# Optimization experiments

Hardware: AMD Instinct MI355X
Metric: run time of the kernel (lower is better)

## Reference

```python
import jax, jax.numpy as jnp
import numpy as np

EMBED_PHI = 1024
EMBED_F = 1024
HIDDEN_F = 1024
N_HEADS = 16
B, S = 2, 2048


def setup_inputs() -> dict:
    key = jax.random.key(0)
    ks = jax.random.split(key, 9)
    sphi = 1.0 / np.sqrt(EMBED_PHI)
    sf = 1.0 / np.sqrt(EMBED_F)
    sh = 1.0 / np.sqrt(HIDDEN_F)
    return {
        "q": jax.random.normal(ks[0], (B, S, EMBED_PHI), jnp.float32),
        "k": jax.random.normal(ks[1], (B, S, EMBED_PHI), jnp.float32),
        "v": jax.random.normal(ks[2], (B, S, EMBED_F), jnp.float32),
        "Wq": jax.random.normal(ks[3], (HIDDEN_F, EMBED_PHI), jnp.float32) * sphi,
        "Wk": jax.random.normal(ks[4], (HIDDEN_F, EMBED_PHI), jnp.float32) * sphi,
        "Wv": jax.random.normal(ks[5], (HIDDEN_F, EMBED_F), jnp.float32) * sf,
        "bv": jax.random.normal(ks[6], (HIDDEN_F,), jnp.float32) * sf,
        "Wo": jax.random.normal(ks[7], (EMBED_F, HIDDEN_F), jnp.float32) * sh,
        "bo": jax.random.normal(ks[8], (EMBED_F,), jnp.float32) * sh,
    }


def reference(q, k, v, Wq, Wk, Wv, bv, Wo, bo):
    Bq, Sq, _ = q.shape
    hd = HIDDEN_F // N_HEADS
    scale = 1.0 / np.sqrt(hd)
    # projections; torch Linear: y = x @ W.T + b
    qh = (q @ Wq.T).reshape(Bq, Sq, N_HEADS, hd).transpose(0, 2, 1, 3)  # [B,H,S,d]
    kh = (k @ Wk.T).reshape(Bq, Sq, N_HEADS, hd).transpose(0, 2, 1, 3)
    vh = (v @ Wv.T + bv).reshape(Bq, Sq, N_HEADS, hd).transpose(0, 2, 1, 3)
    scores = jnp.einsum("bhsd,bhtd->bhst", qh, kh) * scale  # [B,H,S,S]
    # mask: triu(diagonal=0) masked (attend strictly to past) except [0,0] unmasked
    mask = jnp.triu(jnp.ones((Sq, Sq), dtype=bool), k=0).at[0, 0].set(False)
    scores = jnp.where(mask, -jnp.inf, scores)
    probs = jax.nn.softmax(scores, axis=-1)  # dropout is identity at eval
    out = jnp.einsum("bhst,bhtd->bhsd", probs, vh)
    out = out.transpose(0, 2, 1, 3).reshape(Bq, Sq, HIDDEN_F)
    return out @ Wo.T + bo
```

## Files before the change

### kernel.cpp

```cpp
#include <hip/hip_runtime.h>
#include <hip/hip_bf16.h>

typedef __attribute__((ext_vector_type(8))) short short8;
typedef __attribute__((ext_vector_type(4))) float f32x4;
typedef __attribute__((ext_vector_type(4))) unsigned short us4;
typedef __attribute__((ext_vector_type(2))) unsigned int u32x2;

#define NE  1024
#define SEQ 2048

__device__ __forceinline__ float bf2f(unsigned short u) {
    union { unsigned u; float f; } x; x.u = ((unsigned)u) << 16; return x.f;
}
__device__ __forceinline__ unsigned short f2bf(float f) {
    union { float f; unsigned u; } x; x.f = f;
    unsigned r = x.u + 0x7FFFu + ((x.u >> 16) & 1u);
    return (unsigned short)(r >> 16);
}
__device__ __forceinline__ unsigned short f2bf_fast(float f) {
    union { float f; unsigned u; } x; x.f = f;
    return (unsigned short)((x.u + 0x8000u) >> 16);
}

__global__ void detect_dtype(const unsigned short* __restrict__ s,
                             int* __restrict__ flag) {
    __shared__ int cnt;
    const int t = threadIdx.x;
    if (t == 0) cnt = 0;
    __syncthreads();
    unsigned short u = s[t];
    int e = (u >> 7) & 0xFF;
    int sane = (e == 0) || (e >= 100 && e <= 140);
    atomicAdd(&cnt, sane);
    __syncthreads();
    if (t == 0) flag[0] = (cnt >= 230) ? 1 : 0;
}

struct Ptrs7 { const void* s[7]; unsigned short* d[7]; };

__global__ void convert7(Ptrs7 p, const int* __restrict__ flag, int zoff) {
    const int z = blockIdx.z + zoff;
    const int n = (z < 3) ? (4 << 20) : (1 << 20);
    const bool in_f32 = (flag[0] == 0);
    unsigned short* d = p.d[z];
    const int stride = gridDim.x * blockDim.x;
    for (int i8 = blockIdx.x * blockDim.x + threadIdx.x; i8 * 8 < n; i8 += stride) {
        size_t off = (size_t)i8 * 8;
        if (in_f32) {
            const float* sp = (const float*)p.s[z] + off;
            float4 a = *(const float4*)sp, b2 = *(const float4*)(sp + 4);
            short8 sv;
            sv[0] = (short)f2bf(a.x);  sv[1] = (short)f2bf(a.y);
            sv[2] = (short)f2bf(a.z);  sv[3] = (short)f2bf(a.w);
            sv[4] = (short)f2bf(b2.x); sv[5] = (short)f2bf(b2.y);
            sv[6] = (short)f2bf(b2.z); sv[7] = (short)f2bf(b2.w);
            *(short8*)(d + off) = sv;
        } else {
            *(short8*)(d + off) = *(const short8*)((const unsigned short*)p.s[z] + off);
        }
    }
}

template<int AWS, int WWS, int OUTF, int VT>
__global__ __launch_bounds__(256, 3)
void gemm_bt(const void* A0, const void* A1, const void* A2,
             const void* W0, const void* W1, const void* W2,
             const void* b0, const void* b1, const void* b2,
             void* C0, void* C1, void* C2,
             const int* __restrict__ flag)
{
    __shared__ __align__(16) unsigned short As[128 * 32];
    __shared__ __align__(16) unsigned short Bs[128 * 32];
    const int z = blockIdx.z;
    const void* Ap = (z == 0) ? A0 : (z == 1) ? A1 : A2;
    const void* Wp = (z == 0) ? W0 : (z == 1) ? W1 : W2;
    const void* bp = (z == 0) ? b0 : (z == 1) ? b1 : b2;
    void*       Cp = (z == 0) ? C0 : (z == 1) ? C1 : C2;
    const bool in_f32 = (flag[0] == 0);
    const int t = threadIdx.x;
    const int w = t >> 6, l = t & 63, q = l >> 4, n = l & 15;
    const int m0 = blockIdx.y * 128, n0 = blockIdx.x * 128;
    const int wm = (w >> 1) * 64, wn = (w & 1) * 64;
    const int srow = t >> 2, sk = (t & 3) * 8;

    f32x4 acc[4][4] = {};

    for (int k0 = 0; k0 < NE; k0 += 32) {
        if (AWS || !in_f32) {
            #pragma unroll
            for (int hh = 0; hh < 2; hh++) {
                const unsigned short* ga = (const unsigned short*)Ap +
                    (size_t)(m0 + srow + hh * 64) * NE + k0 + sk;
                __builtin_amdgcn_global_load_lds(
                    (const __attribute__((address_space(1))) void*)ga,
                    (__attribute__((address_space(3))) void*)&As[hh * 2048 + w * 512],
                    16, 0, 0);
            }
        } else {
            #pragma unroll
            for (int hh = 0; hh < 2; hh++) {
                const float* a = (const float*)Ap +
                                 (size_t)(m0 + srow + hh * 64) * NE + k0 + sk;
                float4 x0 = *(const float4*)a, x1 = *(const float4*)(a + 4);
                short8 sv;
                sv[0] = (short)f2bf(x0.x); sv[1] = (short)f2bf(x0.y);
                sv[2] = (short)f2bf(x0.z); sv[3] = (short)f2bf(x0.w);
                sv[4] = (short)f2bf(x1.x); sv[5] = (short)f2bf(x1.y);
                sv[6] = (short)f2bf(x1.z); sv[7] = (short)f2bf(x1.w);
                *(short8*)(&As[hh * 2048 + t * 8]) = sv;
            }
        }
        if (WWS || !in_f32) {
            #pragma unroll
            for (int hh = 0; hh < 2; hh++) {
                const unsigned short* ga = (const unsigned short*)Wp +
                    (size_t)(n0 + srow + hh * 64) * NE + k0 + sk;
                __builtin_amdgcn_global_load_lds(
                    (const __attribute__((address_space(1))) void*)ga,
                    (__attribute__((address_space(3))) void*)&Bs[hh * 2048 + w * 512],
                    16, 0, 0);
            }
        } else {
            #pragma unroll
            for (int hh = 0; hh < 2; hh++) {
                const float* a = (const float*)Wp +
                                 (size_t)(n0 + srow + hh * 64) * NE + k0 + sk;
                float4 x0 = *(const float4*)a, x1 = *(const float4*)(a + 4);
                short8 sv;
                sv[0] = (short)f2bf(x0.x); sv[1] = (short)f2bf(x0.y);
                sv[2] = (short)f2bf(x0.z); sv[3] = (short)f2bf(x0.w);
                sv[4] = (short)f2bf(x1.x); sv[5] = (short)f2bf(x1.y);
                sv[6] = (short)f2bf(x1.z); sv[7] = (short)f2bf(x1.w);
                *(short8*)(&Bs[hh * 2048 + t * 8]) = sv;
            }
        }
        __syncthreads();

        short8 af[4], bfv[4];
        #pragma unroll
        for (int mt = 0; mt < 4; mt++)
            af[mt] = *(const short8*)(&As[(wm + mt * 16 + n) * 32 + q * 8]);
        #pragma unroll
        for (int nt = 0; nt < 4; nt++)
            bfv[nt] = *(const short8*)(&Bs[(wn + nt * 16 + n) * 32 + q * 8]);
        #pragma unroll
        for (int mt = 0; mt < 4; mt++)
            #pragma unroll
            for (int nt = 0; nt < 4; nt++)
                acc[mt][nt] = __builtin_amdgcn_mfma_f32_16x16x32_bf16(
                    af[mt], bfv[nt], acc[mt][nt], 0, 0, 0);
        __syncthreads();
    }

    #pragma unroll
    for (int mt = 0; mt < 4; mt++)
        #pragma unroll
        for (int nt = 0; nt < 4; nt++) {
            int row0 = m0 + wm + mt * 16 + q * 4;
            int col  = n0 + wn + nt * 16 + n;
            float bia = 0.f;
            if (bp)
                bia = in_f32 ? ((const float*)bp)[col]
                             : bf2f(((const unsigned short*)bp)[col]);
            if (VT && z == 2) {
                int bb = row0 >> 11, s0 = row0 & 2047;
                int hh2 = col >> 6, dd = col & 63;
                us4 pk4;
                #pragma unroll
                for (int r = 0; r < 4; r++)
                    pk4[r] = f2bf(acc[mt][nt][r] + bia);
                *(us4*)((unsigned short*)Cp +
                        ((size_t)((bb * 16 + hh2) * 64 + dd) << 11) + s0) = pk4;
            } else {
                #pragma unroll
                for (int r = 0; r < 4; r++) {
                    float v2 = acc[mt][nt][r] + bia;
                    size_t idx = (size_t)(row0 + r) * NE + col;
                    if (OUTF && in_f32) ((float*)Cp)[idx] = v2;
                    else                ((unsigned short*)Cp)[idx] = f2bf(v2);
                }
            }
        }
}

__global__ __launch_bounds__(512, 4)
void attn(const unsigned short* qh, const unsigned short* kh,
          const unsigned short* vt, unsigned short* ctx)
{
    __shared__ __align__(16) unsigned short Ks[2][64 * 72];
    __shared__ __align__(16) unsigned short Vt[2][64 * 72];
    __shared__ __align__(16) unsigned short Ps[8][16 * 72];
    const int t = threadIdx.x, w = t >> 6, l = t & 63;
    const int q = l >> 4, n = l & 15;
    const int half = w >> 2, sub = w & 3;
    const int h = blockIdx.y, b = blockIdx.z;
    const int pair = b ? (15 - blockIdx.x) : blockIdx.x;
    const int qbB = pair, qbA = 31 - pair;
    const int qb = half ? qbB : qbA;
    const size_t base = (size_t)b * SEQ * NE + h * 64;
    const size_t vbase = (size_t)((b * 16 + h) * 64) << 11;
    const int i0 = qb * 64 + sub * 16;

    short8 qf[2];
    qf[0] = *(const short8*)(&qh[base + (size_t)(i0 + n) * NE + q * 8]);
    qf[1] = *(const short8*)(&qh[base + (size_t)(i0 + n) * NE + 32 + q * 8]);

    f32x4 o[4] = {};
    float lsp[4] = {0.f, 0.f, 0.f, 0.f};

    const float K1 = 0.125f * 1.4426950408889634f;
    const float B2 = 24.0f * 1.4426950408889634f;

    const int kr = t >> 3, kc = (t & 7) * 8;
    const int vd = t >> 3, vj = (t & 7) * 8;

    short8 pk, pv;
    pk = *(const short8*)(&kh[base + (size_t)kr * NE + kc]);
    pv = *(const short8*)(&vt[vbase + ((size_t)vd << 11) + vj]);
    *(short8*)(&Ks[0][kr * 72 + kc]) = pk;
    *(short8*)(&Vt[0][vd * 72 + vj]) = pv;
    if (qbA >= 1) {
        pk = *(const short8*)(&kh[base + (size_t)(64 + kr) * NE + kc]);
        pv = *(const short8*)(&vt[vbase + ((size_t)vd << 11) + 64 + vj]);
    }
    __syncthreads();

    unsigned short* PsW = &Ps[w][0];
    int cur = 0;

    for (int jt = 0; jt <= qbA; jt++) {
        if (jt + 1 <= qbA) {
            *(short8*)(&Ks[cur ^ 1][kr * 72 + kc]) = pk;
            *(short8*)(&Vt[cur ^ 1][vd * 72 + vj]) = pv;
        }
        if (jt + 2 <= qbA) {
            const int jn = (jt + 2) * 64;
            pk = *(const short8*)(&kh[base + (size_t)(jn + kr) * NE + kc]);
            pv = *(const short8*)(&vt[vbase + ((size_t)vd << 11) + jn + vj]);
        }

        if (jt <= qb) {
            const unsigned short* Kc = &Ks[cur][0];
            const unsigned short* Vc = &Vt[cur][0];
            f32x4 sa[4] = {};
            __builtin_amdgcn_s_setprio(1);
            #pragma unroll
            for (int ks = 0; ks < 2; ks++)
                #pragma unroll
                for (int nt = 0; nt < 4; nt++) {
                    short8 kf = *(const short8*)(&Kc[(nt * 16 + n) * 72 + ks * 32 + q * 8]);
                    sa[nt] = __builtin_amdgcn_mfma_f32_16x16x32_bf16(kf, qf[ks], sa[nt], 0, 0, 0);
                }
            __builtin_amdgcn_s_setprio(0);

            const bool diag = (jt == qb);
            const int i = i0 + n;
            #pragma unroll
            for (int nt = 0; nt < 4; nt++) {
                float p[4];
                #pragma unroll
                for (int r = 0; r < 4; r++) {
                    float e = fmaf(sa[nt][r], K1, -B2);
                    if (diag) {
                        int j = jt * 64 + nt * 16 + q * 4 + r;
                        bool ok = (j < i) || (i == 0 && j == 0);
                        e = ok ? e : -256.0f;
                    }
                    p[r] = __builtin_amdgcn_exp2f(e);
                }
                lsp[nt] += (p[0] + p[1]) + (p[2] + p[3]);
                unsigned w0, w1;
                asm("v_cvt_pk_bf16_f32 %0, %1, %2" : "=v"(w0) : "v"(p[0]), "v"(p[1]));
                asm("v_cvt_pk_bf16_f32 %0, %1, %2" : "=v"(w1) : "v"(p[2]), "v"(p[3]));
                u32x2 wv; wv[0] = w0; wv[1] = w1;
                *(u32x2*)(&PsW[n * 72 + nt * 16 + q * 4]) = wv;
            }
            asm volatile("s_waitcnt lgkmcnt(0)" ::: "memory");

            #pragma unroll
            for (int ks = 0; ks < 2; ks++) {
                short8 pf = *(const short8*)(&PsW[n * 72 + ks * 32 + q * 8]);
                __builtin_amdgcn_s_setprio(1);
                #pragma unroll
                for (int dt = 0; dt < 4; dt++) {
                    short8 vf = *(const short8*)(&Vc[(dt * 16 + n) * 72 + ks * 32 + q * 8]);
                    o[dt] = __builtin_amdgcn_mfma_f32_16x16x32_bf16(pf, vf, o[dt], 0, 0, 0);
                }
                __builtin_amdgcn_s_setprio(0);
            }
        }
        __syncthreads();
        cur ^= 1;
    }

    float ls = (lsp[0] + lsp[1]) + (lsp[2] + lsp[3]);
    ls += __shfl_xor(ls, 16, 64);
    ls += __shfl_xor(ls, 32, 64);

    #pragma unroll
    for (int r = 0; r < 4; r++) {
        float inv = 1.0f / __shfl(ls, q * 4 + r, 64);
        #pragma unroll
        for (int dt = 0; dt < 4; dt++)
            ctx[base + (size_t)(i0 + q * 4 + r) * NE + dt * 16 + n] =
                f2bf(o[dt][r] * inv);
    }
}

extern "C" void kernel_launch(void* const* d_in, const int* in_sizes, int n_in,
                              void* d_out, int out_size, void* d_ws, size_t ws_size,
                              hipStream_t stream) {
    const void* q  = d_in[0];
    const void* k  = d_in[1];
    const void* v  = d_in[2];
    const void* Wq = d_in[3];
    const void* Wk = d_in[4];
    const void* Wv = d_in[5];
    const void* bv = d_in[6];
    const void* Wo = d_in[7];
    const void* bo = d_in[8];

    const size_t MB = 1024 * 1024;
    const size_t M4 = 4 * MB;
    unsigned short* ws = (unsigned short*)d_ws;
    unsigned short* qh  = ws;
    unsigned short* kh  = ws + 1 * M4;
    unsigned short* vt  = ws + 2 * M4;
    unsigned short* ctx = qh;

    int tier = (ws_size >= 56 * MB + 64) ? 2 : (ws_size >= 32 * MB + 64) ? 1 : 0;

    unsigned short *qc, *kc, *vc, *Wqc, *Wkc, *Wvc, *Woc;
    int* flag;
    if (tier == 2) {
        qc = ws + 3 * M4; kc = ws + 4 * M4; vc = ws + 5 * M4;
        Wqc = ws + 6 * M4;           Wkc = Wqc + 1 * MB;
        Wvc = Wqc + 2 * MB;          Woc = Wqc + 3 * MB;
        flag = (int*)((char*)d_ws + 56 * MB);
    } else if (tier == 1) {
        qc = kc = vc = nullptr;
        Wqc = ws + 3 * M4;           Wkc = Wqc + 1 * MB;
        Wvc = Wqc + 2 * MB;          Woc = Wqc + 3 * MB;
        flag = (int*)((char*)d_ws + 32 * MB);
    } else {
        qc = kc = vc = nullptr; Wqc = Wkc = Wvc = Woc = nullptr;
        flag = (int*)((char*)d_ws + 24 * MB);
    }

    detect_dtype<<<1, 256, 0, stream>>>((const unsigned short*)q, flag);

    if (tier > 0) {
        Ptrs7 p;
        p.s[0] = q;  p.s[1] = k;  p.s[2] = v;
        p.s[3] = Wq; p.s[4] = Wk; p.s[5] = Wv; p.s[6] = Wo;
        p.d[0] = qc; p.d[1] = kc; p.d[2] = vc;
        p.d[3] = Wqc; p.d[4] = Wkc; p.d[5] = Wvc; p.d[6] = Woc;
        if (tier == 2)
            convert7<<<dim3(512, 1, 7), 256, 0, stream>>>(p, flag, 0);
        else
            convert7<<<dim3(512, 1, 4), 256, 0, stream>>>(p, flag, 3);
    }

    if (tier == 2)
        gemm_bt<1, 1, 0, 1><<<dim3(8, 32, 3), 256, 0, stream>>>(
            qc, kc, vc, Wqc, Wkc, Wvc, nullptr, nullptr, bv, qh, kh, vt, flag);
    else if (tier == 1)
        gemm_bt<0, 1, 0, 1><<<dim3(8, 32, 3), 256, 0, stream>>>(
            q, k, v, Wqc, Wkc, Wvc, nullptr, nullptr, bv, qh, kh, vt, flag);
    else
        gemm_bt<0, 0, 0, 1><<<dim3(8, 32, 3), 256, 0, stream>>>(
            q, k, v, Wq, Wk, Wv, nullptr, nullptr, bv, qh, kh, vt, flag);

    attn<<<dim3(16, 16, 2), 512, 0, stream>>>(qh, kh, vt, ctx);

    if (tier > 0)
        gemm_bt<1, 1, 1, 0><<<dim3(8, 32, 1), 256, 0, stream>>>(
            ctx, ctx, ctx, Woc, Woc, Woc, bo, bo, bo, d_out, d_out, d_out, flag);
    else
        gemm_bt<1, 0, 1, 0><<<dim3(8, 32, 1), 256, 0, stream>>>(
            ctx, ctx, ctx, Wo, Wo, Wo, bo, bo, bo, d_out, d_out, d_out, flag);
}
```

Before: 228.4 us.

## Software-pipeline attention PV MFMAs and narrow output GEMM tile to 64 columns

In the attention kernel, each iteration now preloads its K fragments up front and defers the P·V MFMAs to the next iteration. The previous tile's P and V fragments are held in registers, so those MFMAs can overlap the next score computation and softmax. A flush runs at jt == qb+1 for the shorter half and after the loop for the longer half. The output projection GEMM gets a TN template parameter and launches with 64-wide N tiles, doubling the block count to fill more CUs. The cost is extra register pressure from the held fragments and less reuse of the A tile in the output GEMM.

```diff
diff --git a/kernel.cpp b/kernel.cpp
--- a/kernel.cpp
+++ b/kernel.cpp
@@ -61,7 +61,7 @@
     }
 }
 
-template<int AWS, int WWS, int OUTF, int VT>
+template<int AWS, int WWS, int OUTF, int VT, int TN = 128>
 __global__ __launch_bounds__(256, 3)
 void gemm_bt(const void* A0, const void* A1, const void* A2,
              const void* W0, const void* W1, const void* W2,
@@ -69,8 +69,9 @@
              void* C0, void* C1, void* C2,
              const int* __restrict__ flag)
 {
+    constexpr int NT = TN / 32;
     __shared__ __align__(16) unsigned short As[128 * 32];
-    __shared__ __align__(16) unsigned short Bs[128 * 32];
+    __shared__ __align__(16) unsigned short Bs[TN * 32];
     const int z = blockIdx.z;
     const void* Ap = (z == 0) ? A0 : (z == 1) ? A1 : A2;
     const void* Wp = (z == 0) ? W0 : (z == 1) ? W1 : W2;
@@ -79,11 +80,11 @@
     const bool in_f32 = (flag[0] == 0);
     const int t = threadIdx.x;
     const int w = t >> 6, l = t & 63, q = l >> 4, n = l & 15;
-    const int m0 = blockIdx.y * 128, n0 = blockIdx.x * 128;
-    const int wm = (w >> 1) * 64, wn = (w & 1) * 64;
+    const int m0 = blockIdx.y * 128, n0 = blockIdx.x * TN;
+    const int wm = (w >> 1) * 64, wn = (w & 1) * (TN / 2);
     const int srow = t >> 2, sk = (t & 3) * 8;
 
-    f32x4 acc[4][4] = {};
+    f32x4 acc[4][NT] = {};
 
     for (int k0 = 0; k0 < NE; k0 += 32) {
         if (AWS || !in_f32) {
@@ -112,7 +113,7 @@
         }
         if (WWS || !in_f32) {
             #pragma unroll
-            for (int hh = 0; hh < 2; hh++) {
+            for (int hh = 0; hh < TN / 64; hh++) {
                 const unsigned short* ga = (const unsigned short*)Wp +
                     (size_t)(n0 + srow + hh * 64) * NE + k0 + sk;
                 __builtin_amdgcn_global_load_lds(
@@ -122,7 +123,7 @@
             }
         } else {
             #pragma unroll
-            for (int hh = 0; hh < 2; hh++) {
+            for (int hh = 0; hh < TN / 64; hh++) {
                 const float* a = (const float*)Wp +
                                  (size_t)(n0 + srow + hh * 64) * NE + k0 + sk;
                 float4 x0 = *(const float4*)a, x1 = *(const float4*)(a + 4);
@@ -136,17 +137,17 @@
         }
         __syncthreads();
 
-        short8 af[4], bfv[4];
+        short8 af[4], bfv[NT];
         #pragma unroll
         for (int mt = 0; mt < 4; mt++)
             af[mt] = *(const short8*)(&As[(wm + mt * 16 + n) * 32 + q * 8]);
         #pragma unroll
-        for (int nt = 0; nt < 4; nt++)
+        for (int nt = 0; nt < NT; nt++)
             bfv[nt] = *(const short8*)(&Bs[(wn + nt * 16 + n) * 32 + q * 8]);
         #pragma unroll
         for (int mt = 0; mt < 4; mt++)
             #pragma unroll
-            for (int nt = 0; nt < 4; nt++)
+            for (int nt = 0; nt < NT; nt++)
                 acc[mt][nt] = __builtin_amdgcn_mfma_f32_16x16x32_bf16(
                     af[mt], bfv[nt], acc[mt][nt], 0, 0, 0);
         __syncthreads();
@@ -155,7 +156,7 @@
     #pragma unroll
     for (int mt = 0; mt < 4; mt++)
         #pragma unroll
-        for (int nt = 0; nt < 4; nt++) {
+        for (int nt = 0; nt < NT; nt++) {
             int row0 = m0 + wm + mt * 16 + q * 4;
             int col  = n0 + wn + nt * 16 + n;
             float bia = 0.f;
@@ -207,6 +208,8 @@
 
     f32x4 o[4] = {};
     float lsp[4] = {0.f, 0.f, 0.f, 0.f};
+    short8 pf_prev[2];
+    short8 vf_prev[8];
 
     const float K1 = 0.125f * 1.4426950408889634f;
     const float B2 = 24.0f * 1.4426950408889634f;
@@ -242,15 +245,33 @@
         if (jt <= qb) {
             const unsigned short* Kc = &Ks[cur][0];
             const unsigned short* Vc = &Vt[cur][0];
+
+            short8 kf[2][4];
+            #pragma unroll
+            for (int ks = 0; ks < 2; ks++)
+                #pragma unroll
+                for (int nt = 0; nt < 4; nt++)
+                    kf[ks][nt] = *(const short8*)(&Kc[(nt * 16 + n) * 72 + ks * 32 + q * 8]);
+
+            if (jt > 0) {
+                __builtin_amdgcn_s_setprio(1);
+                #pragma unroll
+                for (int ks = 0; ks < 2; ks++)
+                    #pragma unroll
+                    for (int dt = 0; dt < 4; dt++)
+                        o[dt] = __builtin_amdgcn_mfma_f32_16x16x32_bf16(
+                            pf_prev[ks], vf_prev[ks * 4 + dt], o[dt], 0, 0, 0);
+                __builtin_amdgcn_s_setprio(0);
+            }
+
             f32x4 sa[4] = {};
             __builtin_amdgcn_s_setprio(1);
             #pragma unroll
             for (int ks = 0; ks < 2; ks++)
                 #pragma unroll
-                for (int nt = 0; nt < 4; nt++) {
-                    short8 kf = *(const short8*)(&Kc[(nt * 16 + n) * 72 + ks * 32 + q * 8]);
-                    sa[nt] = __builtin_amdgcn_mfma_f32_16x16x32_bf16(kf, qf[ks], sa[nt], 0, 0, 0);
-                }
+                for (int nt = 0; nt < 4; nt++)
+                    sa[nt] = __builtin_amdgcn_mfma_f32_16x16x32_bf16(
+                        kf[ks][nt], qf[ks], sa[nt], 0, 0, 0);
             __builtin_amdgcn_s_setprio(0);
 
             const bool diag = (jt == qb);
@@ -278,19 +299,35 @@
             asm volatile("s_waitcnt lgkmcnt(0)" ::: "memory");
 
             #pragma unroll
-            for (int ks = 0; ks < 2; ks++) {
-                short8 pf = *(const short8*)(&PsW[n * 72 + ks * 32 + q * 8]);
-                __builtin_amdgcn_s_setprio(1);
-                #pragma unroll
-                for (int dt = 0; dt < 4; dt++) {
-                    short8 vf = *(const short8*)(&Vc[(dt * 16 + n) * 72 + ks * 32 + q * 8]);
-                    o[dt] = __builtin_amdgcn_mfma_f32_16x16x32_bf16(pf, vf, o[dt], 0, 0, 0);
-                }
-                __builtin_amdgcn_s_setprio(0);
-            }
+            for (int ks = 0; ks < 2; ks++)
+                pf_prev[ks] = *(const short8*)(&PsW[n * 72 + ks * 32 + q * 8]);
+            #pragma unroll
+            for (int ks = 0; ks < 2; ks++)
+                #pragma unroll
+                for (int dt = 0; dt < 4; dt++)
+                    vf_prev[ks * 4 + dt] =
+                        *(const short8*)(&Vc[(dt * 16 + n) * 72 + ks * 32 + q * 8]);
+        } else if (jt == qb + 1) {
+            __builtin_amdgcn_s_setprio(1);
+            #pragma unroll
+            for (int ks = 0; ks < 2; ks++)
+                #pragma unroll
+                for (int dt = 0; dt < 4; dt++)
+                    o[dt] = __builtin_amdgcn_mfma_f32_16x16x32_bf16(
+                        pf_prev[ks], vf_prev[ks * 4 + dt], o[dt], 0, 0, 0);
+            __builtin_amdgcn_s_setprio(0);
         }
         __syncthreads();
         cur ^= 1;
+    }
+
+    if (!half) {
+        #pragma unroll
+        for (int ks = 0; ks < 2; ks++)
+            #pragma unroll
+            for (int dt = 0; dt < 4; dt++)
+                o[dt] = __builtin_amdgcn_mfma_f32_16x16x32_bf16(
+                    pf_prev[ks], vf_prev[ks * 4 + dt], o[dt], 0, 0, 0);
     }
 
     float ls = (lsp[0] + lsp[1]) + (lsp[2] + lsp[3]);
@@ -374,9 +411,9 @@
     attn<<<dim3(16, 16, 2), 512, 0, stream>>>(qh, kh, vt, ctx);
 
     if (tier > 0)
-        gemm_bt<1, 1, 1, 0><<<dim3(8, 32, 1), 256, 0, stream>>>(
+        gemm_bt<1, 1, 1, 0, 64><<<dim3(16, 32, 1), 256, 0, stream>>>(
             ctx, ctx, ctx, Woc, Woc, Woc, bo, bo, bo, d_out, d_out, d_out, flag);
     else
-        gemm_bt<1, 0, 1, 0><<<dim3(8, 32, 1), 256, 0, stream>>>(
+        gemm_bt<1, 0, 1, 0, 64><<<dim3(16, 32, 1), 256, 0, stream>>>(
             ctx, ctx, ctx, Wo, Wo, Wo, bo, bo, bo, d_out, d_out, d_out, flag);
 }
```

Result: faster. 219.6 us (-3.9%).
